# Kernel optimization log

Measured on AMD Instinct MI355X. Metric: run time of the kernel, lower is better.

## Reference

```python
import jax, jax.numpy as jnp
import numpy as np

N_FFT = 512
HOP = 128
WIN = 512
BATCH = 32
N_SAMPLES = 480000


def make_forward_basis():
    n_freq = N_FFT // 2 + 1  # 257
    # periodic hann window (torch.hann_window default periodic=True)
    n = np.arange(WIN, dtype=np.float32)
    window = 0.5 * (1.0 - np.cos(2.0 * np.pi * n / WIN))
    freqs = np.linspace(0.0, N_FFT // 2, n_freq, dtype=np.float32)  # [n_freq]
    t = np.arange(WIN, dtype=np.float32)
    phase = 2.0 * np.pi * freqs[:, None] * t[None, :] / N_FFT
    real = np.cos(phase) * window[None, :]
    imag = -np.sin(phase) * window[None, :]
    basis = np.concatenate([real, imag], axis=0)[:, None, :]
    return jnp.asarray(basis, dtype=jnp.float32)


def setup_inputs() -> dict:
    key = jax.random.key(0)
    x = jax.random.normal(key, (BATCH, N_SAMPLES), dtype=jnp.float32)
    return {"x": x, "forward_basis": make_forward_basis()}


def reference(x, forward_basis):
    # x: [B, T] -> [B, 1, T]
    x = x[:, None, :]
    pad = N_FFT // 2
    x_padded = jnp.pad(x, ((0, 0), (0, 0), (pad, pad)), mode="reflect")
    # single conv over concatenated real+imag basis: [B, 2*n_freq, n_frames]
    spec = jax.lax.conv_general_dilated(
        x_padded, forward_basis,
        window_strides=(HOP,), padding="VALID",
        dimension_numbers=("NCH", "OIH", "NCH"))
    n_freq = N_FFT // 2 + 1
    real_spec = spec[:, :n_freq, :]
    imag_spec = spec[:, n_freq:, :]
    return jnp.sqrt(real_spec ** 2 + imag_spec ** 2)
```

## Files before the change

### kernel.cpp

```cpp
#include <hip/hip_runtime.h>

#define NFREQ   257
#define NFRAMES 3751
#define NS      480000
#define HOP     128
#define WIN     512

#define NB      32
#define BN      128
#define NFT     30
#define STEPS   32
#define XWPITCH 272
#define XW_B    35632
#define AHALF   16384
#define WNYQ_B  1024
#define XGROUPS 2096

typedef __attribute__((ext_vector_type(8))) short short8;
typedef __attribute__((ext_vector_type(4))) float f32x4;

__device__ __forceinline__ short f2bf(float f) {
    __bf16 b = (__bf16)f;
    return __builtin_bit_cast(short, b);
}
__device__ __forceinline__ float bf2f(short s) {
    unsigned int u = ((unsigned int)(unsigned short)s) << 16;
    return __builtin_bit_cast(float, u);
}
__device__ __forceinline__ void gload_lds16(const void* g, void* l) {
    __builtin_amdgcn_global_load_lds(
        (const __attribute__((address_space(1))) void*)g,
        (__attribute__((address_space(3))) void*)l, 16, 0, 0);
}

__global__ __launch_bounds__(256)
void prep_basis4(const float* __restrict__ basis,
                 short* __restrict__ abL, short* __restrict__ wnyqG) {
    int g = blockIdx.x * 256 + threadIdx.x;
    if (g < 32768) {
        int ob   = g * 16;
        int step = ob >> 14;
        int rem  = ob & 16383;
        int pl   = rem >> 13;
        int r    = (rem >> 7) & 63;
        int s    = (rem >> 4) & 7;
        int u    = s ^ (r & 7);
        int f    = r + (u >> 2) * 64;
        int kg   = u & 3;
        int fp   = step >> 4;
        int ks32 = step & 15;
        int row  = pl * NFREQ + fp * 128 + f;
        int k0   = ks32 * 32 + kg * 8;
        const float4* p = reinterpret_cast<const float4*>(
            basis + (size_t)row * WIN + k0);
        float4 a0 = p[0], a1 = p[1];
        short8 v;
        v[0]=f2bf(a0.x); v[1]=f2bf(a0.y); v[2]=f2bf(a0.z); v[3]=f2bf(a0.w);
        v[4]=f2bf(a1.x); v[5]=f2bf(a1.y); v[6]=f2bf(a1.z); v[7]=f2bf(a1.w);
        *reinterpret_cast<short8*>(reinterpret_cast<char*>(abL) + ob) = v;
    } else if (g < 32832) {
        int j = g - 32768;
        const float4* p = reinterpret_cast<const float4*>(basis + (size_t)256 * WIN + j * 8);
        float4 a0 = p[0], a1 = p[1];
        short8 v;
        v[0]=f2bf(a0.x); v[1]=f2bf(a0.y); v[2]=f2bf(a0.z); v[3]=f2bf(a0.w);
        v[4]=f2bf(a1.x); v[5]=f2bf(a1.y); v[6]=f2bf(a1.z); v[7]=f2bf(a1.w);
        *reinterpret_cast<short8*>(wnyqG + j * 8) = v;
    }
}

__global__ __launch_bounds__(256, 2)
void stft_mfma_kernel(const float* __restrict__ x,
                      const short* __restrict__ abL,
                      const short* __restrict__ wnyqG,
                      float* __restrict__ out)
{
    __shared__ __align__(16) char smem[XW_B + 2 * AHALF + WNYQ_B];
    char* const xw   = smem;
    char* const aBuf = smem + XW_B;
    char* const wnyq = smem + XW_B + 2 * AHALF;

    const int tid  = threadIdx.x;
    const int wave = tid >> 6;
    const int lane = tid & 63;
    const int lgrp = lane >> 4;
    const int l15  = lane & 15;

    const int logical = (blockIdx.x & 7) * 120 + (blockIdx.x >> 3);
    const int ft = logical % NFT;
    const int b  = logical / NFT;
    const int t0 = ft * BN;

    const char* abLc = (const char*)abL;

    #pragma unroll
    for (int i = 0; i < 4; ++i) {
        int c = wave * 4 + i;
        gload_lds16(abLc + c * 1024 + lane * 16, aBuf + c * 1024);
    }
    if (wave == 0)
        gload_lds16((const char*)wnyqG + lane * 16, wnyq);

    {
        const float* __restrict__ xb = x + (size_t)b * NS;
        const int sbase = t0 * 128 - 256;
        #pragma unroll
        for (int i = 0; i < 9; ++i) {
            int g = tid + i * 256;
            if (g < XGROUPS) {
                int ix = sbase + g * 8;
                short8 v;
                if (ix >= 0 && ix + 8 <= NS) {
                    const float4* p = reinterpret_cast<const float4*>(xb + ix);
                    float4 a0 = p[0], a1 = p[1];
                    v[0]=f2bf(a0.x); v[1]=f2bf(a0.y); v[2]=f2bf(a0.z); v[3]=f2bf(a0.w);
                    v[4]=f2bf(a1.x); v[5]=f2bf(a1.y); v[6]=f2bf(a1.z); v[7]=f2bf(a1.w);
                } else {
                    #pragma unroll
                    for (int q = 0; q < 8; ++q) {
                        int idx = ix + q;
                        if (idx < 0) idx = -idx;
                        if (idx >= NS + 256) { v[q] = 0; continue; }
                        if (idx >= NS) idx = 2 * NS - 2 - idx;
                        v[q] = f2bf(xb[idx]);
                    }
                }
                *reinterpret_cast<short8*>(xw + (g >> 4) * XWPITCH + (g & 15) * 16) = v;
            }
        }
    }

    f32x4 accR[2][8], accI[2][8];
    #pragma unroll
    for (int m = 0; m < 2; ++m)
        #pragma unroll
        for (int n = 0; n < 8; ++n) {
            accR[m][n] = f32x4{0.f,0.f,0.f,0.f};
            accI[m][n] = f32x4{0.f,0.f,0.f,0.f};
        }

    const int rb = (wave & 1) * 32 + l15;
    const int ub = (wave >> 1) * 4 + lgrp;

    #pragma unroll 1
    for (int s = 0; s < STEPS; ++s) {
        asm volatile("s_waitcnt vmcnt(0)" ::: "memory");
        __builtin_amdgcn_sched_barrier(0);
        __syncthreads();
        __builtin_amdgcn_sched_barrier(0);

        char* const aCur = aBuf + (s & 1) * AHALF;

        if (s + 1 < STEPS) {
            char* const aNxt = aBuf + ((s + 1) & 1) * AHALF;
            const char* sb = abLc + (size_t)(s + 1) * AHALF;
            #pragma unroll
            for (int i = 0; i < 4; ++i) {
                int c = wave * 4 + i;
                gload_lds16(sb + c * 1024 + lane * 16, aNxt + c * 1024);
            }
        }
        __builtin_amdgcn_sched_barrier(0);

        const int ks32 = s & 15;
        short8 aRv[2], aIv[2], xv[8];
        #pragma unroll
        for (int m = 0; m < 2; ++m) {
            int r   = rb + m * 16;
            int off = r * 128 + ((ub ^ (r & 7)) << 4);
            aRv[m] = *reinterpret_cast<const short8*>(aCur + off);
            aIv[m] = *reinterpret_cast<const short8*>(aCur + 8192 + off);
        }
        {
            int r8 = ks32 * 64 + lgrp * 16;
            int T  = r8 + ((r8 >> 8) << 4);
            const char* xwl = xw + l15 * XWPITCH + T;
            #pragma unroll
            for (int nt = 0; nt < 8; ++nt)
                xv[nt] = *reinterpret_cast<const short8*>(xwl + nt * (16 * XWPITCH));
        }
        #pragma unroll
        for (int m = 0; m < 2; ++m)
            #pragma unroll
            for (int nt = 0; nt < 8; ++nt) {
                accR[m][nt] = __builtin_amdgcn_mfma_f32_16x16x32_bf16(aRv[m], xv[nt], accR[m][nt], 0, 0, 0);
                accI[m][nt] = __builtin_amdgcn_mfma_f32_16x16x32_bf16(aIv[m], xv[nt], accI[m][nt], 0, 0, 0);
            }

        if ((s & 15) == 15) {
            const int fp = s >> 4;
            float* ob = out + (size_t)b * NFREQ * NFRAMES;
            const int fb = fp * 128 + wave * 32 + lgrp * 4;
            const int tb = t0 + l15;
            #pragma unroll
            for (int m = 0; m < 2; ++m)
                #pragma unroll
                for (int nt = 0; nt < 8; ++nt) {
                    int t = tb + nt * 16;
                    if (t < NFRAMES) {
                        #pragma unroll
                        for (int r = 0; r < 4; ++r) {
                            int f = fb + m * 16 + r;
                            float vr = accR[m][nt][r], vi = accI[m][nt][r];
                            ob[(size_t)f * NFRAMES + t] = sqrtf(vr * vr + vi * vi);
                        }
                    }
                    accR[m][nt] = f32x4{0.f,0.f,0.f,0.f};
                    accI[m][nt] = f32x4{0.f,0.f,0.f,0.f};
                }
        }
    }

    {
        const int fl = wave * 32 + (lane & 31);
        const int h  = lane >> 5;
        const int xbase = (fl + 2 * h) * XWPITCH;
        const int wbase = h * 512;
        float acc = 0.f;
        #pragma unroll
        for (int j = 0; j < 32; ++j) {
            short8 xv8 = *reinterpret_cast<const short8*>(
                xw + xbase + (j >> 4) * XWPITCH + (j & 15) * 16);
            short8 wv8 = *reinterpret_cast<const short8*>(wnyq + wbase + j * 16);
            #pragma unroll
            for (int q = 0; q < 8; ++q)
                acc = fmaf(bf2f(xv8[q]), bf2f(wv8[q]), acc);
        }
        acc += __shfl_xor(acc, 32);
        int t = t0 + fl;
        if (h == 0 && t < NFRAMES)
            out[((size_t)b * NFREQ + 256) * NFRAMES + t] = fabsf(acc);
    }
}

extern "C" void kernel_launch(void* const* d_in, const int* in_sizes, int n_in,
                              void* d_out, int out_size, void* d_ws, size_t ws_size,
                              hipStream_t stream) {
    const float* x     = (const float*)d_in[0];
    const float* basis = (const float*)d_in[1];
    float* out = (float*)d_out;

    short* abL   = (short*)d_ws;
    short* wnyqG = abL + 262144;

    prep_basis4<<<dim3(129), 256, 0, stream>>>(basis, abL, wnyqG);
    stft_mfma_kernel<<<dim3(NFT * NB), 256, 0, stream>>>(x, abL, wnyqG, out);
}
```

Before: 87.58 us.

## Enlarge STFT block tile to 256 frames with 8 waves and triple-buffered basis

Each block now covers 256 frames instead of 128, using 512 threads arranged as a 2x4 wave grid. Each wave computes a 64-frequency by 64-frame tile, so each loaded A and x fragment feeds more MFMAs and the overlapping reflect-padded window is staged once per larger tile. The basis staging goes from double to triple buffering with a partial vmcnt wait and a new 64-byte-row swizzled layout. MFMA issue is wrapped in setprio. The larger LDS footprint (about 120KB) likely limits the kernel to one block per CU, and with half as many blocks the tail and load-balance behaviour changes.

```diff
diff --git a/kernel.cpp b/kernel.cpp
--- a/kernel.cpp
+++ b/kernel.cpp
@@ -7,14 +7,14 @@
 #define WIN     512
 
 #define NB      32
-#define BN      128
-#define NFT     30
+#define BN      256
+#define NFT     15
 #define STEPS   32
 #define XWPITCH 272
-#define XW_B    35632
-#define AHALF   16384
+#define XW_B    70448
+#define ASTEP   16384
 #define WNYQ_B  1024
-#define XGROUPS 2096
+#define XGROUPS 4144
 
 typedef __attribute__((ext_vector_type(8))) short short8;
 typedef __attribute__((ext_vector_type(4))) float f32x4;
@@ -34,7 +34,7 @@
 }
 
 __global__ __launch_bounds__(256)
-void prep_basis4(const float* __restrict__ basis,
+void prep_basis5(const float* __restrict__ basis,
                  short* __restrict__ abL, short* __restrict__ wnyqG) {
     int g = blockIdx.x * 256 + threadIdx.x;
     if (g < 32768) {
@@ -42,17 +42,13 @@
         int step = ob >> 14;
         int rem  = ob & 16383;
         int pl   = rem >> 13;
-        int r    = (rem >> 7) & 63;
-        int s    = (rem >> 4) & 7;
-        int u    = s ^ (r & 7);
-        int f    = r + (u >> 2) * 64;
-        int kg   = u & 3;
-        int fp   = step >> 4;
-        int ks32 = step & 15;
-        int row  = pl * NFREQ + fp * 128 + f;
-        int k0   = ks32 * 32 + kg * 8;
+        int row  = (rem >> 6) & 127;
+        int slot = (rem >> 4) & 3;
+        int kg   = slot ^ ((row >> 2) & 3);
+        int fr   = (step >> 4) * 128 + row;
+        int k0   = (step & 15) * 32 + kg * 8;
         const float4* p = reinterpret_cast<const float4*>(
-            basis + (size_t)row * WIN + k0);
+            basis + ((size_t)(pl * NFREQ + fr)) * WIN + k0);
         float4 a0 = p[0], a1 = p[1];
         short8 v;
         v[0]=f2bf(a0.x); v[1]=f2bf(a0.y); v[2]=f2bf(a0.z); v[3]=f2bf(a0.w);
@@ -69,44 +65,38 @@
     }
 }
 
-__global__ __launch_bounds__(256, 2)
+__global__ __launch_bounds__(512, 2)
 void stft_mfma_kernel(const float* __restrict__ x,
                       const short* __restrict__ abL,
                       const short* __restrict__ wnyqG,
                       float* __restrict__ out)
 {
-    __shared__ __align__(16) char smem[XW_B + 2 * AHALF + WNYQ_B];
+    __shared__ __align__(16) char smem[XW_B + 3 * ASTEP + WNYQ_B];
     char* const xw   = smem;
     char* const aBuf = smem + XW_B;
-    char* const wnyq = smem + XW_B + 2 * AHALF;
+    char* const wnyq = smem + XW_B + 3 * ASTEP;
 
     const int tid  = threadIdx.x;
     const int wave = tid >> 6;
     const int lane = tid & 63;
+    const int wr   = wave >> 2;
+    const int wc   = wave & 3;
     const int lgrp = lane >> 4;
     const int l15  = lane & 15;
 
-    const int logical = (blockIdx.x & 7) * 120 + (blockIdx.x >> 3);
+    const int logical = (blockIdx.x & 7) * 60 + (blockIdx.x >> 3);
     const int ft = logical % NFT;
     const int b  = logical / NFT;
     const int t0 = ft * BN;
 
     const char* abLc = (const char*)abL;
 
-    #pragma unroll
-    for (int i = 0; i < 4; ++i) {
-        int c = wave * 4 + i;
-        gload_lds16(abLc + c * 1024 + lane * 16, aBuf + c * 1024);
-    }
-    if (wave == 0)
-        gload_lds16((const char*)wnyqG + lane * 16, wnyq);
-
     {
         const float* __restrict__ xb = x + (size_t)b * NS;
         const int sbase = t0 * 128 - 256;
         #pragma unroll
         for (int i = 0; i < 9; ++i) {
-            int g = tid + i * 256;
+            int g = tid + i * 512;
             if (g < XGROUPS) {
                 int ix = sbase + g * 8;
                 short8 v;
@@ -129,73 +119,86 @@
             }
         }
     }
-
-    f32x4 accR[2][8], accI[2][8];
+    if (wave == 0)
+        gload_lds16((const char*)wnyqG + lane * 16, wnyq);
     #pragma unroll
-    for (int m = 0; m < 2; ++m)
-        #pragma unroll
-        for (int n = 0; n < 8; ++n) {
+    for (int st = 0; st < 2; ++st) {
+        const char* sb = abLc + (size_t)st * ASTEP;
+        char* dst = aBuf + st * ASTEP;
+        int c = wave * 2;
+        gload_lds16(sb + c * 1024 + lane * 16, dst + c * 1024);
+        gload_lds16(sb + (c + 1) * 1024 + lane * 16, dst + (c + 1) * 1024);
+    }
+    __syncthreads();
+
+    f32x4 accR[4][4], accI[4][4];
+    #pragma unroll
+    for (int m = 0; m < 4; ++m)
+        #pragma unroll
+        for (int n = 0; n < 4; ++n) {
             accR[m][n] = f32x4{0.f,0.f,0.f,0.f};
             accI[m][n] = f32x4{0.f,0.f,0.f,0.f};
         }
 
-    const int rb = (wave & 1) * 32 + l15;
-    const int ub = (wave >> 1) * 4 + lgrp;
+    const int aSlot = (lgrp ^ (l15 >> 2)) << 4;
+    const int aRow0 = wr * 64 + l15;
 
     #pragma unroll 1
     for (int s = 0; s < STEPS; ++s) {
-        asm volatile("s_waitcnt vmcnt(0)" ::: "memory");
+        if ((s & 15) == 0) {
+            asm volatile("s_waitcnt vmcnt(0)" ::: "memory");
+        } else {
+            asm volatile("s_waitcnt vmcnt(2)" ::: "memory");
+        }
+        asm volatile("s_waitcnt lgkmcnt(0)" ::: "memory");
         __builtin_amdgcn_sched_barrier(0);
-        __syncthreads();
+        __builtin_amdgcn_s_barrier();
         __builtin_amdgcn_sched_barrier(0);
 
-        char* const aCur = aBuf + (s & 1) * AHALF;
-
-        if (s + 1 < STEPS) {
-            char* const aNxt = aBuf + ((s + 1) & 1) * AHALF;
-            const char* sb = abLc + (size_t)(s + 1) * AHALF;
-            #pragma unroll
-            for (int i = 0; i < 4; ++i) {
-                int c = wave * 4 + i;
-                gload_lds16(sb + c * 1024 + lane * 16, aNxt + c * 1024);
-            }
+        if (s + 2 < STEPS) {
+            const char* sb = abLc + (size_t)(s + 2) * ASTEP;
+            char* dst = aBuf + ((s + 2) % 3) * ASTEP;
+            int c = wave * 2;
+            gload_lds16(sb + c * 1024 + lane * 16, dst + c * 1024);
+            gload_lds16(sb + (c + 1) * 1024 + lane * 16, dst + (c + 1) * 1024);
         }
         __builtin_amdgcn_sched_barrier(0);
 
+        const char* aCur = aBuf + (s % 3) * ASTEP;
         const int ks32 = s & 15;
-        short8 aRv[2], aIv[2], xv[8];
-        #pragma unroll
-        for (int m = 0; m < 2; ++m) {
-            int r   = rb + m * 16;
-            int off = r * 128 + ((ub ^ (r & 7)) << 4);
+        short8 aRv[4], aIv[4], xv[4];
+        #pragma unroll
+        for (int m = 0; m < 4; ++m) {
+            int off = (aRow0 + m * 16) * 64 + aSlot;
             aRv[m] = *reinterpret_cast<const short8*>(aCur + off);
             aIv[m] = *reinterpret_cast<const short8*>(aCur + 8192 + off);
         }
         {
-            int r8 = ks32 * 64 + lgrp * 16;
-            int T  = r8 + ((r8 >> 8) << 4);
-            const char* xwl = xw + l15 * XWPITCH + T;
-            #pragma unroll
-            for (int nt = 0; nt < 8; ++nt)
+            int flat0 = (wc * 64 + l15) * 256 + ks32 * 64 + lgrp * 16;
+            const char* xwl = xw + flat0 + ((flat0 >> 8) << 4);
+            #pragma unroll
+            for (int nt = 0; nt < 4; ++nt)
                 xv[nt] = *reinterpret_cast<const short8*>(xwl + nt * (16 * XWPITCH));
         }
-        #pragma unroll
-        for (int m = 0; m < 2; ++m)
-            #pragma unroll
-            for (int nt = 0; nt < 8; ++nt) {
+        __builtin_amdgcn_s_setprio(1);
+        #pragma unroll
+        for (int m = 0; m < 4; ++m)
+            #pragma unroll
+            for (int nt = 0; nt < 4; ++nt) {
                 accR[m][nt] = __builtin_amdgcn_mfma_f32_16x16x32_bf16(aRv[m], xv[nt], accR[m][nt], 0, 0, 0);
                 accI[m][nt] = __builtin_amdgcn_mfma_f32_16x16x32_bf16(aIv[m], xv[nt], accI[m][nt], 0, 0, 0);
             }
+        __builtin_amdgcn_s_setprio(0);
 
         if ((s & 15) == 15) {
             const int fp = s >> 4;
             float* ob = out + (size_t)b * NFREQ * NFRAMES;
-            const int fb = fp * 128 + wave * 32 + lgrp * 4;
-            const int tb = t0 + l15;
-            #pragma unroll
-            for (int m = 0; m < 2; ++m)
+            const int fb = fp * 128 + wr * 64 + lgrp * 4;
+            const int tb = t0 + wc * 64 + l15;
+            #pragma unroll
+            for (int m = 0; m < 4; ++m)
                 #pragma unroll
-                for (int nt = 0; nt < 8; ++nt) {
+                for (int nt = 0; nt < 4; ++nt) {
                     int t = tb + nt * 16;
                     if (t < NFRAMES) {
                         #pragma unroll
@@ -243,6 +246,6 @@
     short* abL   = (short*)d_ws;
     short* wnyqG = abL + 262144;
 
-    prep_basis4<<<dim3(129), 256, 0, stream>>>(basis, abL, wnyqG);
-    stft_mfma_kernel<<<dim3(NFT * NB), 256, 0, stream>>>(x, abL, wnyqG, out);
-}
+    prep_basis5<<<dim3(129), 256, 0, stream>>>(basis, abL, wnyqG);
+    stft_mfma_kernel<<<dim3(NFT * NB), 512, 0, stream>>>(x, abL, wnyqG, out);
+}
```

Measured after the change: 101.1 us. 1.15x slower.
